# Optimization experiments

Hardware: AMD Instinct MI355X
Metric: run time of the kernel (lower is better)

## Reference

```python
import jax, jax.numpy as jnp
import numpy as np

HEADS = 16
HEAD_DIM = 32
WINDOW = 64  # kernel_size = 2*WINDOW + 1 = 129
NEG = -1e30


def setup_inputs() -> dict:
    key = jax.random.key(0)
    ks = jax.random.split(key, 9)
    B, T, D, G = 4, 8192, HEADS * HEAD_DIM, 64
    x = jax.random.normal(ks[0], (B, T, D), jnp.float32)
    def W(k):
        return jax.random.normal(k, (D, D), jnp.float32) * 0.02
    def b(k):
        return jax.random.normal(k, (D,), jnp.float32) * 0.02
    return {
        "x": x,
        "Wq": W(ks[1]), "bq": b(ks[2]),
        "Wk": W(ks[3]), "bk": b(ks[4]),
        "Wv": W(ks[5]), "bv": b(ks[6]),
        "Wo": W(ks[7]), "bo": b(ks[8]),
        "global_idx": jnp.arange(G, dtype=jnp.int64 if jax.config.jax_enable_x64 else jnp.int32),
    }


def _sparse_global_attn(x, Wq, bq, Wk, bk, Wv, bv, Wo, bo, global_idx):
    B, T, D = x.shape
    H, d, w = HEADS, HEAD_DIM, WINDOW
    scale = 1.0 / (d ** 0.5)

    def proj(W, b):
        # (B,T,D) -> (B,H,T,d)
        return (x @ W + b).reshape(B, T, H, d).transpose(0, 2, 1, 3)

    q, k, v = proj(Wq, bq), proj(Wk, bk), proj(Wv, bv)

    offsets = jnp.arange(-w, w + 1)  # (K,)
    K = offsets.shape[0]

    # Local band scores: score[b,h,t,j] = <q[t], k[t+offset_j]>, computed
    # offset-by-offset via roll to avoid a (B,H,T,K,d) gather.
    def score_step(_, o):
        s = jnp.einsum('bhtd,bhtd->bht', q, jnp.roll(k, -o, axis=2))
        return None, s
    _, loc = jax.lax.scan(score_step, None, offsets)  # (K,B,H,T)
    loc = jnp.moveaxis(loc, 0, -1) * scale            # (B,H,T,K)

    pos = jnp.arange(T)[:, None] + offsets[None, :]   # (T,K)
    valid = (pos >= 0) & (pos < T)
    loc = jnp.where(valid[None, None], loc, NEG)

    # Global-token scores (global tokens shared across the batch)
    k_g = k[:, :, global_idx, :]                      # (B,H,G,d)
    v_g = v[:, :, global_idx, :]
    gsc = jnp.einsum('bhtd,bhgd->bhtg', q, k_g) * scale  # (B,H,T,G)

    # Joint softmax over [local window | global tokens] (duplicates where a
    # global token lies inside the local window, matching the original).
    attn = jax.nn.softmax(jnp.concatenate([loc, gsc], axis=-1), axis=-1)
    a_loc = jnp.moveaxis(attn[..., :K], -1, 0)        # (K,B,H,T)
    a_g = attn[..., K:]                               # (B,H,T,G)

    def ctx_step(acc, oa):
        o, a = oa
        return acc + a[..., None] * jnp.roll(v, -o, axis=2), None
    ctx, _ = jax.lax.scan(ctx_step, jnp.zeros_like(q), (offsets, a_loc))
    ctx = ctx + jnp.einsum('bhtg,bhgd->bhtd', a_g, v_g)  # (B,H,T,d)

    out = ctx.transpose(0, 2, 1, 3).reshape(B, T, D)
    return out @ Wo + bo


def reference(x, Wq, bq, Wk, bk, Wv, bv, Wo, bo, global_idx):
    return _sparse_global_attn(x, Wq, bq, Wk, bk, Wv, bv, Wo, bo, global_idx)
```

## Files before the change

### kernel.cpp

```cpp
#include <hip/hip_runtime.h>
#include <hip/hip_bf16.h>
#include <cstdint>
#include <cstddef>

using bf16 = __hip_bfloat16;
typedef __bf16 bf16x8 __attribute__((ext_vector_type(8)));
typedef __bf16 bf16x4 __attribute__((ext_vector_type(4)));
typedef float f32x4 __attribute__((ext_vector_type(4)));

constexpr int BB = 4;
constexpr int TS = 8192;
constexpr int NH = 16;
constexpr int HD = 32;
constexpr int DM = 512;
constexpr int NQKV = 1536;
constexpr int NG = 64;

#define MFMA16(a, b, c) __builtin_amdgcn_mfma_f32_16x16x32_bf16((a), (b), (c), 0, 0, 0)

__device__ __forceinline__ bf16x8 ld8(const bf16* p) { return *(const bf16x8*)p; }
__device__ __forceinline__ bf16x4 ld4(const bf16* p) { return *(const bf16x4*)p; }
__device__ __forceinline__ unsigned short b16bits(bf16 v) { return __builtin_bit_cast(unsigned short, v); }

__device__ __forceinline__ void gl_lds16(const bf16* g, void* l) {
  __builtin_amdgcn_global_load_lds((const __attribute__((address_space(1))) void*)g,
                                   (__attribute__((address_space(3))) void*)l, 16, 0, 0);
}

__global__ void prep_kernel(const float* __restrict__ x,
                            const float* __restrict__ Wq, const float* __restrict__ bq,
                            const float* __restrict__ Wk, const float* __restrict__ bk,
                            const float* __restrict__ Wv, const float* __restrict__ bv,
                            const float* __restrict__ Wo,
                            bf16* __restrict__ xb, bf16* __restrict__ Wp,
                            bf16* __restrict__ Wp2, float* __restrict__ bqkv) {
  const int64_t stride = (int64_t)gridDim.x * blockDim.x;
  const int64_t i0 = (int64_t)blockIdx.x * blockDim.x + threadIdx.x;
  const float4* x4 = (const float4*)x;
  ushort4* xb4 = (ushort4*)xb;
  for (int64_t i = i0; i < (int64_t)BB * TS * DM / 4; i += stride) {
    float4 v = x4[i];
    ushort4 o;
    o.x = b16bits(__float2bfloat16(v.x));
    o.y = b16bits(__float2bfloat16(v.y));
    o.z = b16bits(__float2bfloat16(v.z));
    o.w = b16bits(__float2bfloat16(v.w));
    xb4[i] = o;
  }
  for (int64_t c = i0; c < (int64_t)NQKV * DM / 8; c += stride) {
    const int lane = (int)(c & 63), f = (int)((c >> 6) & 3), ks = (int)((c >> 8) & 1);
    const int kt = (int)((c >> 9) & 7), wn = (int)((c >> 12) & 1), nt = (int)(c >> 13);
    const int n = nt * 128 + wn * 64 + f * 16 + (lane & 15);
    const int k = kt * 64 + ks * 32 + (lane >> 4) * 8;
    const float* W = (n < 512) ? Wq : ((n < 1024) ? Wk : Wv);
    const int nn = n & 511;
    #pragma unroll
    for (int j = 0; j < 8; ++j)
      Wp[c * 8 + j] = __float2bfloat16(W[(size_t)(k + j) * DM + nn]);
  }
  for (int64_t c = i0; c < (int64_t)DM * DM / 8; c += stride) {
    const int lane = (int)(c & 63), f = (int)((c >> 6) & 3), ks = (int)((c >> 8) & 1);
    const int kt = (int)((c >> 9) & 7), wn = (int)((c >> 12) & 1), nt = (int)(c >> 13);
    const int n = nt * 128 + wn * 64 + f * 16 + (lane & 15);
    const int k = kt * 64 + ks * 32 + (lane >> 4) * 8;
    #pragma unroll
    for (int j = 0; j < 8; ++j)
      Wp2[c * 8 + j] = __float2bfloat16(Wo[(size_t)(k + j) * DM + n]);
  }
  for (int64_t i = i0; i < NQKV; i += stride)
    bqkv[i] = (i < 512) ? bq[i] : ((i < 1024) ? bk[i - 512] : bv[i - 1024]);
}

template <bool F32OUT, bool WVT>
__global__ __launch_bounds__(256, 3) void gemm_bias(const bf16* __restrict__ A,
                                                    const bf16* __restrict__ Bp,
                                                    const float* __restrict__ bias,
                                                    void* __restrict__ Cv,
                                                    bf16* __restrict__ vt,
                                                    int M, int N, int K, int cpx) {
  __shared__ __attribute__((aligned(16))) char smem[35072];
  const int tid = threadIdx.x;
  const int lane = tid & 63, wid = tid >> 6;
  const int grp = lane >> 4, col = lane & 15;
  const int bid = (blockIdx.x & 7) * cpx + (blockIdx.x >> 3);
  const int NT = N >> 7;
  const int mt = bid / NT, nt = bid % NT;
  const int m0 = mt << 7, n0 = nt << 7;
  const int wm = wid >> 1, wn = wid & 1;
  const int KT = K >> 6;
  f32x4 acc[4][4] = {};

  const bf16* bp = Bp + (size_t)(nt * 2 + wn) * KT * 4096 + lane * 8;
  bf16x8 breg[2][4];
  auto loadB = [&](int kt) {
    #pragma unroll
    for (int ks = 0; ks < 2; ++ks)
      #pragma unroll
      for (int f = 0; f < 4; ++f)
        breg[ks][f] = ld8(bp + (size_t)(kt * 8 + ks * 4 + f) * 512);
  };
  auto stageA = [&](int kt) {
    char* buf = smem + (kt & 1) * 16384;
    #pragma unroll
    for (int c = 0; c < 4; ++c) {
      const int chunk = wid * 4 + c;
      const int row = chunk * 8 + (lane >> 3);
      const int sl = lane & 7;
      const int koff = ((sl ^ (row & 7)) << 3) + (kt << 6);
      gl_lds16(A + (size_t)(m0 + row) * K + koff, buf + chunk * 1024);
    }
  };

  stageA(0);
  loadB(0);
  for (int kt = 0; kt < KT; ++kt) {
    if (kt + 1 < KT) {
      stageA(kt + 1);
      __builtin_amdgcn_sched_barrier(0);
      asm volatile("s_waitcnt vmcnt(4)" ::: "memory");
    } else {
      __builtin_amdgcn_sched_barrier(0);
      asm volatile("s_waitcnt vmcnt(0)" ::: "memory");
    }
    __builtin_amdgcn_sched_barrier(0);
    __builtin_amdgcn_s_barrier();
    __builtin_amdgcn_sched_barrier(0);
    const char* sA = smem + (kt & 1) * 16384;
    #pragma unroll
    for (int ks = 0; ks < 2; ++ks) {
      bf16x8 af[4];
      #pragma unroll
      for (int f = 0; f < 4; ++f) {
        const int ra = wm * 64 + f * 16 + col;
        af[f] = *(const bf16x8*)(sA + ra * 128 + (((ks * 4 + grp) ^ (ra & 7)) << 4));
      }
      #pragma unroll
      for (int i = 0; i < 4; ++i)
        #pragma unroll
        for (int j = 0; j < 4; ++j)
          acc[i][j] = MFMA16(af[i], breg[ks][j], acc[i][j]);
    }
    if (kt + 1 < KT) loadB(kt + 1);
    __builtin_amdgcn_sched_barrier(0);
    __builtin_amdgcn_s_barrier();
    __builtin_amdgcn_sched_barrier(0);
  }

  const bool wv = WVT && (n0 >= 1024);
  if (!wv) {
    #pragma unroll
    for (int i = 0; i < 4; ++i)
      #pragma unroll
      for (int j = 0; j < 4; ++j) {
        const int n = n0 + wn * 64 + j * 16 + col;
        const float bz = bias[n];
        #pragma unroll
        for (int r = 0; r < 4; ++r) {
          const int m = m0 + wm * 64 + i * 16 + grp * 4 + r;
          const float v = acc[i][j][r] + bz;
          if (F32OUT)
            ((float*)Cv)[(size_t)m * N + n] = v;
          else
            ((bf16*)Cv)[(size_t)m * N + n] = __float2bfloat16(v);
        }
      }
  } else {
    __syncthreads();
    bf16* lt = (bf16*)smem;
    #pragma unroll
    for (int i = 0; i < 4; ++i)
      #pragma unroll
      for (int j = 0; j < 4; ++j) {
        const int nl = wn * 64 + j * 16 + col;
        const float bz = bias[n0 + nl];
        #pragma unroll
        for (int r = 0; r < 4; ++r) {
          const int ml = wm * 64 + i * 16 + grp * 4 + r;
          lt[nl * 136 + (ml ^ ((nl & 7) << 4))] = __float2bfloat16(acc[i][j][r] + bz);
        }
      }
    __syncthreads();
    const int row = tid >> 1, half = tid & 1;
    const int b = m0 >> 13, t0 = m0 & 8191;
    bf16* dst = vt + (size_t)(b * DM + (n0 & 511) + row) * TS + t0 + half * 64;
    const bf16* srcl = lt + row * 136;
    #pragma unroll
    for (int c = 0; c < 8; ++c)
      *(bf16x8*)(dst + c * 8) =
          *(const bf16x8*)(srcl + ((half * 64 + c * 8) ^ ((row & 7) << 4)));
  }
}

__global__ void vgt_kernel(const bf16* __restrict__ vt, const int* __restrict__ gidx,
                           bf16* __restrict__ vtp, bf16* __restrict__ vgt) {
  const int64_t stride = (int64_t)gridDim.x * blockDim.x;
  const int64_t i0 = (int64_t)blockIdx.x * blockDim.x + threadIdx.x;
  for (int64_t i = i0; i < 512; i += stride) {
    if (i < 64) vtp[i - 64] = __float2bfloat16(0.f);
    else vtp[(size_t)2048 * TS + (i - 64)] = __float2bfloat16(0.f);
  }
  for (int64_t i = i0; i < (int64_t)2048 * NG; i += stride) {
    const int row = (int)(i >> 6), g = (int)(i & 63);
    const int gi = gidx[g];
    vgt[i] = vt[(size_t)row * TS + gi];
  }
}

__global__ __launch_bounds__(256) void attn_kernel(const bf16* __restrict__ qkv,
                                                   const bf16* __restrict__ vt,
                                                   const bf16* __restrict__ vgt,
                                                   const int* __restrict__ gidx,
                                                   bf16* __restrict__ ctx) {
  constexpr int VST = 216;
  constexpr int VGST = 88;
  __shared__ __attribute__((aligned(16))) char smem[35840];
  bf16* sV = (bf16*)smem;
  bf16* sVg = (bf16*)(smem + 13824);
  bf16* sK = (bf16*)(smem + 19456);
  bf16* sKg = (bf16*)(smem + 31744);

  const int tid = threadIdx.x, wid = tid >> 6, lane = tid & 63;
  const int grp = lane >> 4, col = lane & 15;
  const int bid = (blockIdx.x & 7) * 1024 + (blockIdx.x >> 3);
  const int tile = bid & 127, h = (bid >> 7) & 15, b = bid >> 11;
  const int t0b = tile * 64;
  const int kbb = t0b - 64;
  const int bh = b * NH + h;
  const bf16* base = qkv + (size_t)b * TS * NQKV;
  const bf16* kpl = base + 512 + h * 32;

  #pragma unroll
  for (int it = 0; it < 3; ++it) {
    const int idx = it * 256 + tid;
    const int row = idx >> 2, part = idx & 3;
    const int tok = min(max(kbb + row, 0), TS - 1);
    gl_lds16(kpl + (size_t)tok * NQKV + ((part ^ (row & 3)) << 3), sK + idx * 8);
  }
  {
    const int row = tid >> 2, part = tid & 3;
    const int gi = gidx[row];
    gl_lds16(kpl + (size_t)gi * NQKV + ((part ^ (row & 3)) << 3), sKg + tid * 8);
  }
  {
    const bf16* vr = vt + (size_t)(bh * HD + (tid >> 3)) * TS + kbb;
    #pragma unroll
    for (int i = 0; i < 4; ++i) {
      const int c = i * 8 + (tid & 7);
      if (c < 27) *(bf16x8*)(sV + (tid >> 3) * VST + c * 8) = ld8(vr + c * 8);
    }
  }
  {
    const int row = tid >> 3, c = tid & 7;
    *(bf16x8*)(sVg + row * VGST + c * 8) = ld8(vgt + (size_t)(bh * HD + row) * NG + c * 8);
  }
  __syncthreads();

  const int qt = t0b + wid * 16;
  const int offw = wid * 16;

  const bf16x8 qf = ld8(base + (size_t)(qt + col) * NQKV + h * 32 + grp * 8);
  const f32x4 z = {0.f, 0.f, 0.f, 0.f};
  f32x4 s[13];
  #pragma unroll
  for (int f = 0; f < 9; ++f) {
    const int row = offw + f * 16 + col;
    bf16x8 kf = ld8(sK + row * 32 + ((grp ^ (row & 3)) << 3));
    s[f] = MFMA16(kf, qf, z);
  }
  #pragma unroll
  for (int f = 0; f < 4; ++f) {
    const int row = f * 16 + col;
    bf16x8 kf = ld8(sKg + row * 32 + ((grp ^ (row & 3)) << 3));
    s[9 + f] = MFMA16(kf, qf, z);
  }
  const float scale = 0.17677669529663688f;
  float mx = -3e38f;
  const bool interior = (tile >= 1) & (tile <= 126);
  if (interior) {
    #pragma unroll
    for (int f = 0; f < 13; ++f) {
      #pragma unroll
      for (int r = 0; r < 4; ++r) {
        float v = s[f][r] * scale;
        if (f == 0) v = (grp * 4 + r >= col) ? v : -1e30f;
        if (f == 8) v = (grp * 4 + r <= col) ? v : -1e30f;
        s[f][r] = v;
        mx = fmaxf(mx, v);
      }
    }
  } else {
    #pragma unroll
    for (int f = 0; f < 13; ++f) {
      #pragma unroll
      for (int r = 0; r < 4; ++r) {
        float v = s[f][r] * scale;
        if (f < 9) {
          const int j = f * 16 + grp * 4 + r;
          const int pos = qt - 64 + j;
          const bool valid = (j >= col) & (j <= col + 128) & (pos >= 0) & (pos < TS);
          v = valid ? v : -1e30f;
        }
        s[f][r] = v;
        mx = fmaxf(mx, v);
      }
    }
  }
  mx = fmaxf(mx, __shfl_xor(mx, 16));
  mx = fmaxf(mx, __shfl_xor(mx, 32));
  float sum = 0.f;
  bf16x8 pb[7];
  #pragma unroll
  for (int f = 0; f < 13; ++f) {
    const int pr = (f < 9) ? (f >> 1) : (5 + ((f - 9) >> 1));
    const int hf = (f < 9) ? (f & 1) : ((f - 9) & 1);
    #pragma unroll
    for (int r = 0; r < 4; ++r) {
      float p = __expf(s[f][r] - mx);
      sum += p;
      pb[pr][hf * 4 + r] = (__bf16)__float2bfloat16(p);
    }
  }
  #pragma unroll
  for (int r = 0; r < 4; ++r) pb[4][4 + r] = (__bf16)__float2bfloat16(0.f);
  sum += __shfl_xor(sum, 16);
  sum += __shfl_xor(sum, 32);
  const float sm = 1.0f / sum;

  f32x4 c0 = z, c1 = z;
  const bf16* sVr0 = sV + col * VST;
  const bf16* sVr1 = sV + (col + 16) * VST;
  #pragma unroll
  for (int i = 0; i < 5; ++i) {
    const int kk = offw + i * 32 + grp * 4;
    bf16x8 a0 = __builtin_shufflevector(ld4(sVr0 + kk), ld4(sVr0 + kk + 16),
                                        0, 1, 2, 3, 4, 5, 6, 7);
    bf16x8 a1 = __builtin_shufflevector(ld4(sVr1 + kk), ld4(sVr1 + kk + 16),
                                        0, 1, 2, 3, 4, 5, 6, 7);
    c0 = MFMA16(a0, pb[i], c0);
    c1 = MFMA16(a1, pb[i], c1);
  }
  const bf16* sVg0 = sVg + col * VGST;
  const bf16* sVg1 = sVg + (col + 16) * VGST;
  #pragma unroll
  for (int i = 0; i < 2; ++i) {
    const int kk = i * 32 + grp * 4;
    bf16x8 a0 = __builtin_shufflevector(ld4(sVg0 + kk), ld4(sVg0 + kk + 16),
                                        0, 1, 2, 3, 4, 5, 6, 7);
    bf16x8 a1 = __builtin_shufflevector(ld4(sVg1 + kk), ld4(sVg1 + kk + 16),
                                        0, 1, 2, 3, 4, 5, 6, 7);
    c0 = MFMA16(a0, pb[5 + i], c0);
    c1 = MFMA16(a1, pb[5 + i], c1);
  }
  const int t = qt + col;
  bf16* op = ctx + ((size_t)(b * TS + t)) * DM + h * 32 + grp * 4;
  ushort4 o0, o1;
  o0.x = b16bits(__float2bfloat16(c0[0] * sm));
  o0.y = b16bits(__float2bfloat16(c0[1] * sm));
  o0.z = b16bits(__float2bfloat16(c0[2] * sm));
  o0.w = b16bits(__float2bfloat16(c0[3] * sm));
  o1.x = b16bits(__float2bfloat16(c1[0] * sm));
  o1.y = b16bits(__float2bfloat16(c1[1] * sm));
  o1.z = b16bits(__float2bfloat16(c1[2] * sm));
  o1.w = b16bits(__float2bfloat16(c1[3] * sm));
  *(ushort4*)op = o0;
  *(ushort4*)(op + 16) = o1;
}

extern "C" void kernel_launch(void* const* d_in, const int* in_sizes, int n_in,
                              void* d_out, int out_size, void* d_ws, size_t ws_size,
                              hipStream_t stream) {
  (void)in_sizes; (void)n_in; (void)out_size; (void)ws_size;
  const float* x = (const float*)d_in[0];
  const float* Wq = (const float*)d_in[1];
  const float* bq = (const float*)d_in[2];
  const float* Wk = (const float*)d_in[3];
  const float* bk = (const float*)d_in[4];
  const float* Wv = (const float*)d_in[5];
  const float* bv = (const float*)d_in[6];
  const float* Wo = (const float*)d_in[7];
  const float* bo = (const float*)d_in[8];
  const int* gidx = (const int*)d_in[9];
  float* out = (float*)d_out;

  char* ws = (char*)d_ws;
  size_t off = 0;
  auto alloc = [&](size_t bytes) -> void* {
    void* p = ws + off;
    off += (bytes + 255) & ~(size_t)255;
    return p;
  };
  bf16* xb = (bf16*)alloc((size_t)BB * TS * DM * 2);
  bf16* Wp = (bf16*)alloc((size_t)NQKV * DM * 2);
  bf16* Wp2 = (bf16*)alloc((size_t)DM * DM * 2);
  float* bqkv = (float*)alloc((size_t)NQKV * 4);
  bf16* qkv = (bf16*)alloc((size_t)BB * TS * NQKV * 2);
  bf16* vta = (bf16*)alloc(((size_t)2048 * TS + 512) * 2);
  bf16* vgt = (bf16*)alloc((size_t)2048 * NG * 2);
  bf16* ctx = xb;
  bf16* vt = vta + 64;

  prep_kernel<<<dim3(2048), dim3(256), 0, stream>>>(x, Wq, bq, Wk, bk, Wv, bv, Wo,
                                                    xb, Wp, Wp2, bqkv);
  gemm_bias<false, true><<<dim3(3072), dim3(256), 0, stream>>>(xb, Wp, bqkv, qkv, vt,
                                                               BB * TS, NQKV, DM, 384);
  vgt_kernel<<<dim3(512), dim3(256), 0, stream>>>(vt, gidx, vt, vgt);
  attn_kernel<<<dim3(8192), dim3(256), 0, stream>>>(qkv, vt, vgt, gidx, ctx);
  gemm_bias<true, false><<<dim3(1024), dim3(256), 0, stream>>>(ctx, Wp2, bo, out, nullptr,
                                                               BB * TS, DM, DM, 128);
}
```

Baseline: 168.0 us.

## Restructure projection GEMMs to 64x512 tiles with full-K A staged in LDS

The projection GEMMs change from 128x128 tiles with double-buffered K-chunks to 64-row by 512-column tiles. Each 512-thread block stages the entire 64x512 A panel into LDS once, then each of eight waves streams its own B columns from global memory, with register double-buffering over 16 k-steps. The weight prepacking layout is changed to match the new per-wave column groups, and the V-transpose epilogue is split into two passes. This cuts A re-reads and per-k barriers, at the cost of 64KB LDS per block, which may limit occupancy, and more B traffic per output.

Result: slower. 194.0 us (+15.5%).

```diff
diff --git a/kernel.cpp b/kernel.cpp
--- a/kernel.cpp
+++ b/kernel.cpp
@@ -49,8 +49,8 @@
   }
   for (int64_t c = i0; c < (int64_t)NQKV * DM / 8; c += stride) {
     const int lane = (int)(c & 63), f = (int)((c >> 6) & 3), ks = (int)((c >> 8) & 1);
-    const int kt = (int)((c >> 9) & 7), wn = (int)((c >> 12) & 1), nt = (int)(c >> 13);
-    const int n = nt * 128 + wn * 64 + f * 16 + (lane & 15);
+    const int kt = (int)((c >> 9) & 7), g = (int)(c >> 12);
+    const int n = g * 64 + f * 16 + (lane & 15);
     const int k = kt * 64 + ks * 32 + (lane >> 4) * 8;
     const float* W = (n < 512) ? Wq : ((n < 1024) ? Wk : Wv);
     const int nn = n & 511;
@@ -60,8 +60,8 @@
   }
   for (int64_t c = i0; c < (int64_t)DM * DM / 8; c += stride) {
     const int lane = (int)(c & 63), f = (int)((c >> 6) & 3), ks = (int)((c >> 8) & 1);
-    const int kt = (int)((c >> 9) & 7), wn = (int)((c >> 12) & 1), nt = (int)(c >> 13);
-    const int n = nt * 128 + wn * 64 + f * 16 + (lane & 15);
+    const int kt = (int)((c >> 9) & 7), g = (int)(c >> 12);
+    const int n = g * 64 + f * 16 + (lane & 15);
     const int k = kt * 64 + ks * 32 + (lane >> 4) * 8;
     #pragma unroll
     for (int j = 0; j < 8; ++j)
@@ -71,123 +71,124 @@
     bqkv[i] = (i < 512) ? bq[i] : ((i < 1024) ? bk[i - 512] : bv[i - 1024]);
 }
 
-template <bool F32OUT, bool WVT>
-__global__ __launch_bounds__(256, 3) void gemm_bias(const bf16* __restrict__ A,
+template <bool F32OUT, bool WVT, int NTB>
+__global__ __launch_bounds__(512, 4) void gemm_bias(const bf16* __restrict__ A,
                                                     const bf16* __restrict__ Bp,
                                                     const float* __restrict__ bias,
                                                     void* __restrict__ Cv,
                                                     bf16* __restrict__ vt,
-                                                    int M, int N, int K, int cpx) {
-  __shared__ __attribute__((aligned(16))) char smem[35072];
+                                                    int M, int N, int cpx) {
+  __shared__ __attribute__((aligned(16))) char smem[65536];
   const int tid = threadIdx.x;
   const int lane = tid & 63, wid = tid >> 6;
   const int grp = lane >> 4, col = lane & 15;
   const int bid = (blockIdx.x & 7) * cpx + (blockIdx.x >> 3);
-  const int NT = N >> 7;
-  const int mt = bid / NT, nt = bid % NT;
-  const int m0 = mt << 7, n0 = nt << 7;
-  const int wm = wid >> 1, wn = wid & 1;
-  const int KT = K >> 6;
+  const int mt = bid / NTB, nt = bid % NTB;
+  const int m0 = mt << 6, n0 = nt << 9;
   f32x4 acc[4][4] = {};
 
-  const bf16* bp = Bp + (size_t)(nt * 2 + wn) * KT * 4096 + lane * 8;
-  bf16x8 breg[2][4];
-  auto loadB = [&](int kt) {
-    #pragma unroll
-    for (int ks = 0; ks < 2; ++ks)
-      #pragma unroll
-      for (int f = 0; f < 4; ++f)
-        breg[ks][f] = ld8(bp + (size_t)(kt * 8 + ks * 4 + f) * 512);
-  };
-  auto stageA = [&](int kt) {
-    char* buf = smem + (kt & 1) * 16384;
-    #pragma unroll
-    for (int c = 0; c < 4; ++c) {
-      const int chunk = wid * 4 + c;
-      const int row = chunk * 8 + (lane >> 3);
-      const int sl = lane & 7;
-      const int koff = ((sl ^ (row & 7)) << 3) + (kt << 6);
-      gl_lds16(A + (size_t)(m0 + row) * K + koff, buf + chunk * 1024);
-    }
-  };
-
-  stageA(0);
-  loadB(0);
-  for (int kt = 0; kt < KT; ++kt) {
-    if (kt + 1 < KT) {
-      stageA(kt + 1);
-      __builtin_amdgcn_sched_barrier(0);
-      asm volatile("s_waitcnt vmcnt(4)" ::: "memory");
-    } else {
-      __builtin_amdgcn_sched_barrier(0);
-      asm volatile("s_waitcnt vmcnt(0)" ::: "memory");
-    }
-    __builtin_amdgcn_sched_barrier(0);
-    __builtin_amdgcn_s_barrier();
-    __builtin_amdgcn_sched_barrier(0);
-    const char* sA = smem + (kt & 1) * 16384;
-    #pragma unroll
-    for (int ks = 0; ks < 2; ++ks) {
+  #pragma unroll
+  for (int it = 0; it < 8; ++it) {
+    const int idx = it * 512 + tid;
+    const int row = idx >> 6, c = idx & 63;
+    const int kt = c >> 3, sl = c & 7;
+    const int koff = kt * 64 + ((sl ^ (row & 7)) << 3);
+    gl_lds16(A + (size_t)(m0 + row) * 512 + koff, smem + idx * 16);
+  }
+  __syncthreads();
+
+  const bf16* bp = Bp + (size_t)(nt * 8 + wid) * 32768 + lane * 8;
+  bf16x8 bA[4], bB[4];
+  #pragma unroll
+  for (int f = 0; f < 4; ++f) bA[f] = ld8(bp + (size_t)f * 512);
+
+  #pragma unroll
+  for (int s = 0; s < 16; s += 2) {
+    if (s + 1 < 16)
+      #pragma unroll
+      for (int f = 0; f < 4; ++f) bB[f] = ld8(bp + (size_t)((s + 1) * 4 + f) * 512);
+    {
+      const int kt = s >> 1, ks = s & 1;
       bf16x8 af[4];
       #pragma unroll
       for (int f = 0; f < 4; ++f) {
-        const int ra = wm * 64 + f * 16 + col;
-        af[f] = *(const bf16x8*)(sA + ra * 128 + (((ks * 4 + grp) ^ (ra & 7)) << 4));
+        const int ra = f * 16 + col;
+        af[f] = *(const bf16x8*)(smem + ra * 1024 + kt * 128 +
+                                 (((ks * 4 + grp) ^ (ra & 7)) << 4));
       }
       #pragma unroll
       for (int i = 0; i < 4; ++i)
         #pragma unroll
         for (int j = 0; j < 4; ++j)
-          acc[i][j] = MFMA16(af[i], breg[ks][j], acc[i][j]);
-    }
-    if (kt + 1 < KT) loadB(kt + 1);
-    __builtin_amdgcn_sched_barrier(0);
-    __builtin_amdgcn_s_barrier();
-    __builtin_amdgcn_sched_barrier(0);
-  }
-
-  const bool wv = WVT && (n0 >= 1024);
+          acc[i][j] = MFMA16(af[i], bA[j], acc[i][j]);
+    }
+    if (s + 2 < 16)
+      #pragma unroll
+      for (int f = 0; f < 4; ++f) bA[f] = ld8(bp + (size_t)((s + 2) * 4 + f) * 512);
+    if (s + 1 < 16) {
+      const int kt = (s + 1) >> 1, ks = (s + 1) & 1;
+      bf16x8 af[4];
+      #pragma unroll
+      for (int f = 0; f < 4; ++f) {
+        const int ra = f * 16 + col;
+        af[f] = *(const bf16x8*)(smem + ra * 1024 + kt * 128 +
+                                 (((ks * 4 + grp) ^ (ra & 7)) << 4));
+      }
+      #pragma unroll
+      for (int i = 0; i < 4; ++i)
+        #pragma unroll
+        for (int j = 0; j < 4; ++j)
+          acc[i][j] = MFMA16(af[i], bB[j], acc[i][j]);
+    }
+  }
+
+  const bool wv = WVT && (nt == 2);
   if (!wv) {
     #pragma unroll
-    for (int i = 0; i < 4; ++i)
-      #pragma unroll
-      for (int j = 0; j < 4; ++j) {
-        const int n = n0 + wn * 64 + j * 16 + col;
-        const float bz = bias[n];
+    for (int j = 0; j < 4; ++j) {
+      const int n = n0 + wid * 64 + j * 16 + col;
+      const float bz = bias[n];
+      #pragma unroll
+      for (int i = 0; i < 4; ++i)
         #pragma unroll
         for (int r = 0; r < 4; ++r) {
-          const int m = m0 + wm * 64 + i * 16 + grp * 4 + r;
+          const int m = m0 + i * 16 + grp * 4 + r;
           const float v = acc[i][j][r] + bz;
           if (F32OUT)
             ((float*)Cv)[(size_t)m * N + n] = v;
           else
             ((bf16*)Cv)[(size_t)m * N + n] = __float2bfloat16(v);
         }
-      }
+    }
   } else {
-    __syncthreads();
     bf16* lt = (bf16*)smem;
-    #pragma unroll
-    for (int i = 0; i < 4; ++i)
-      #pragma unroll
-      for (int j = 0; j < 4; ++j) {
-        const int nl = wn * 64 + j * 16 + col;
-        const float bz = bias[n0 + nl];
+    const int b = m0 >> 13, t0 = m0 & 8191;
+    #pragma unroll
+    for (int p = 0; p < 2; ++p) {
+      __syncthreads();
+      if ((wid >> 2) == p) {
         #pragma unroll
-        for (int r = 0; r < 4; ++r) {
-          const int ml = wm * 64 + i * 16 + grp * 4 + r;
-          lt[nl * 136 + (ml ^ ((nl & 7) << 4))] = __float2bfloat16(acc[i][j][r] + bz);
+        for (int j = 0; j < 4; ++j) {
+          const int nl = (wid & 3) * 64 + j * 16 + col;
+          const float bz = bias[n0 + p * 256 + nl];
+          #pragma unroll
+          for (int i = 0; i < 4; ++i)
+            #pragma unroll
+            for (int r = 0; r < 4; ++r) {
+              const int ml = i * 16 + grp * 4 + r;
+              lt[nl * 72 + (ml ^ ((nl & 7) << 3))] = __float2bfloat16(acc[i][j][r] + bz);
+            }
         }
       }
-    __syncthreads();
-    const int row = tid >> 1, half = tid & 1;
-    const int b = m0 >> 13, t0 = m0 & 8191;
-    bf16* dst = vt + (size_t)(b * DM + (n0 & 511) + row) * TS + t0 + half * 64;
-    const bf16* srcl = lt + row * 136;
-    #pragma unroll
-    for (int c = 0; c < 8; ++c)
-      *(bf16x8*)(dst + c * 8) =
-          *(const bf16x8*)(srcl + ((half * 64 + c * 8) ^ ((row & 7) << 4)));
+      __syncthreads();
+      const int row = tid >> 1, half = tid & 1;
+      bf16* dst = vt + (size_t)(b * DM + p * 256 + row) * TS + t0 + half * 32;
+      const bf16* srcl = lt + row * 72;
+      #pragma unroll
+      for (int c = 0; c < 4; ++c)
+        *(bf16x8*)(dst + c * 8) =
+            *(const bf16x8*)(srcl + ((half * 32 + c * 8) ^ ((row & 7) << 3)));
+    }
   }
 }
 
@@ -401,10 +402,10 @@
 
   prep_kernel<<<dim3(2048), dim3(256), 0, stream>>>(x, Wq, bq, Wk, bk, Wv, bv, Wo,
                                                     xb, Wp, Wp2, bqkv);
-  gemm_bias<false, true><<<dim3(3072), dim3(256), 0, stream>>>(xb, Wp, bqkv, qkv, vt,
-                                                               BB * TS, NQKV, DM, 384);
+  gemm_bias<false, true, 3><<<dim3(1536), dim3(512), 0, stream>>>(
+      xb, Wp, bqkv, qkv, vt, BB * TS, NQKV, 192);
   vgt_kernel<<<dim3(512), dim3(256), 0, stream>>>(vt, gidx, vt, vgt);
   attn_kernel<<<dim3(8192), dim3(256), 0, stream>>>(qkv, vt, vgt, gidx, ctx);
-  gemm_bias<true, false><<<dim3(1024), dim3(256), 0, stream>>>(ctx, Wp2, bo, out, nullptr,
-                                                               BB * TS, DM, DM, 128);
-}
+  gemm_bias<true, false, 1><<<dim3(512), dim3(512), 0, stream>>>(
+      ctx, Wp2, bo, out, nullptr, BB * TS, DM, 64);
+}
```

## Triple-buffer A tiles and double-buffer B registers in GEMM pipeline

Applied to the files above, without the earlier changes.

The GEMM mainloop moves from a double-buffered A tile in LDS to a three-stage ring. A is prefetched two iterations ahead, and B fragments are double-buffered in registers so the next B load is issued before the MFMAs. K is fixed at compile time so the loop fully unrolls, and s_setprio is raised around the MFMA block. The prep-kernel weight packing index math is simplified (g = c>>12), which gives the same layout. LDS grows to 48KB and register use rises, which could lower occupancy under launch_bounds(256,3).

Result: slower. 212.6 us (+26.5%).

```diff
diff --git a/kernel.cpp b/kernel.cpp
--- a/kernel.cpp
+++ b/kernel.cpp
@@ -49,8 +49,8 @@
   }
   for (int64_t c = i0; c < (int64_t)NQKV * DM / 8; c += stride) {
     const int lane = (int)(c & 63), f = (int)((c >> 6) & 3), ks = (int)((c >> 8) & 1);
-    const int kt = (int)((c >> 9) & 7), wn = (int)((c >> 12) & 1), nt = (int)(c >> 13);
-    const int n = nt * 128 + wn * 64 + f * 16 + (lane & 15);
+    const int kt = (int)((c >> 9) & 7), g = (int)(c >> 12);
+    const int n = g * 64 + f * 16 + (lane & 15);
     const int k = kt * 64 + ks * 32 + (lane >> 4) * 8;
     const float* W = (n < 512) ? Wq : ((n < 1024) ? Wk : Wv);
     const int nn = n & 511;
@@ -60,8 +60,8 @@
   }
   for (int64_t c = i0; c < (int64_t)DM * DM / 8; c += stride) {
     const int lane = (int)(c & 63), f = (int)((c >> 6) & 3), ks = (int)((c >> 8) & 1);
-    const int kt = (int)((c >> 9) & 7), wn = (int)((c >> 12) & 1), nt = (int)(c >> 13);
-    const int n = nt * 128 + wn * 64 + f * 16 + (lane & 15);
+    const int kt = (int)((c >> 9) & 7), g = (int)(c >> 12);
+    const int n = g * 64 + f * 16 + (lane & 15);
     const int k = kt * 64 + ks * 32 + (lane >> 4) * 8;
     #pragma unroll
     for (int j = 0; j < 8; ++j)
@@ -77,8 +77,8 @@
                                                     const float* __restrict__ bias,
                                                     void* __restrict__ Cv,
                                                     bf16* __restrict__ vt,
-                                                    int M, int N, int K, int cpx) {
-  __shared__ __attribute__((aligned(16))) char smem[35072];
+                                                    int M, int N, int cpx) {
+  __shared__ __attribute__((aligned(16))) char smem[49152];
   const int tid = threadIdx.x;
   const int lane = tid & 63, wid = tid >> 6;
   const int grp = lane >> 4, col = lane & 15;
@@ -87,60 +87,66 @@
   const int mt = bid / NT, nt = bid % NT;
   const int m0 = mt << 7, n0 = nt << 7;
   const int wm = wid >> 1, wn = wid & 1;
-  const int KT = K >> 6;
+  constexpr int KT = 8;
   f32x4 acc[4][4] = {};
 
-  const bf16* bp = Bp + (size_t)(nt * 2 + wn) * KT * 4096 + lane * 8;
-  bf16x8 breg[2][4];
-  auto loadB = [&](int kt) {
-    #pragma unroll
-    for (int ks = 0; ks < 2; ++ks)
-      #pragma unroll
-      for (int f = 0; f < 4; ++f)
-        breg[ks][f] = ld8(bp + (size_t)(kt * 8 + ks * 4 + f) * 512);
-  };
-  auto stageA = [&](int kt) {
-    char* buf = smem + (kt & 1) * 16384;
+  const bf16* bp = Bp + (size_t)(nt * 2 + wn) * (KT * 4096) + lane * 8;
+  bf16x8 brg[2][2][4];
+
+  auto stageA = [&](int kt, int buf3) {
+    char* buf = smem + buf3 * 16384;
     #pragma unroll
     for (int c = 0; c < 4; ++c) {
       const int chunk = wid * 4 + c;
       const int row = chunk * 8 + (lane >> 3);
       const int sl = lane & 7;
       const int koff = ((sl ^ (row & 7)) << 3) + (kt << 6);
-      gl_lds16(A + (size_t)(m0 + row) * K + koff, buf + chunk * 1024);
+      gl_lds16(A + (size_t)(m0 + row) * 512 + koff, buf + chunk * 1024);
     }
   };
 
-  stageA(0);
-  loadB(0);
+  stageA(0, 0);
+  #pragma unroll
+  for (int ks = 0; ks < 2; ++ks)
+    #pragma unroll
+    for (int f = 0; f < 4; ++f)
+      brg[0][ks][f] = ld8(bp + (size_t)(ks * 4 + f) * 512);
+  stageA(1, 1);
+
+  #pragma unroll
   for (int kt = 0; kt < KT; ++kt) {
-    if (kt + 1 < KT) {
-      stageA(kt + 1);
-      __builtin_amdgcn_sched_barrier(0);
-      asm volatile("s_waitcnt vmcnt(4)" ::: "memory");
-    } else {
-      __builtin_amdgcn_sched_barrier(0);
-      asm volatile("s_waitcnt vmcnt(0)" ::: "memory");
-    }
+    __builtin_amdgcn_sched_barrier(0);
+    if (kt + 1 < KT) asm volatile("s_waitcnt vmcnt(4)" ::: "memory");
+    else             asm volatile("s_waitcnt vmcnt(0)" ::: "memory");
     __builtin_amdgcn_sched_barrier(0);
     __builtin_amdgcn_s_barrier();
     __builtin_amdgcn_sched_barrier(0);
-    const char* sA = smem + (kt & 1) * 16384;
-    #pragma unroll
-    for (int ks = 0; ks < 2; ++ks) {
-      bf16x8 af[4];
+    const char* sA = smem + (kt % 3) * 16384;
+    bf16x8 af[2][4];
+    #pragma unroll
+    for (int ks = 0; ks < 2; ++ks)
       #pragma unroll
       for (int f = 0; f < 4; ++f) {
         const int ra = wm * 64 + f * 16 + col;
-        af[f] = *(const bf16x8*)(sA + ra * 128 + (((ks * 4 + grp) ^ (ra & 7)) << 4));
+        af[ks][f] = *(const bf16x8*)(sA + ra * 128 + (((ks * 4 + grp) ^ (ra & 7)) << 4));
       }
+    if (kt + 1 < KT) {
+      #pragma unroll
+      for (int ks = 0; ks < 2; ++ks)
+        #pragma unroll
+        for (int f = 0; f < 4; ++f)
+          brg[(kt + 1) & 1][ks][f] = ld8(bp + (size_t)((kt + 1) * 8 + ks * 4 + f) * 512);
+    }
+    __builtin_amdgcn_s_setprio(1);
+    #pragma unroll
+    for (int ks = 0; ks < 2; ++ks)
       #pragma unroll
       for (int i = 0; i < 4; ++i)
         #pragma unroll
         for (int j = 0; j < 4; ++j)
-          acc[i][j] = MFMA16(af[i], breg[ks][j], acc[i][j]);
-    }
-    if (kt + 1 < KT) loadB(kt + 1);
+          acc[i][j] = MFMA16(af[ks][i], brg[kt & 1][ks][j], acc[i][j]);
+    __builtin_amdgcn_s_setprio(0);
+    if (kt + 2 < KT) stageA(kt + 2, (kt + 2) % 3);
     __builtin_amdgcn_sched_barrier(0);
     __builtin_amdgcn_s_barrier();
     __builtin_amdgcn_sched_barrier(0);
@@ -402,9 +408,9 @@
   prep_kernel<<<dim3(2048), dim3(256), 0, stream>>>(x, Wq, bq, Wk, bk, Wv, bv, Wo,
                                                     xb, Wp, Wp2, bqkv);
   gemm_bias<false, true><<<dim3(3072), dim3(256), 0, stream>>>(xb, Wp, bqkv, qkv, vt,
-                                                               BB * TS, NQKV, DM, 384);
+                                                               BB * TS, NQKV, 384);
   vgt_kernel<<<dim3(512), dim3(256), 0, stream>>>(vt, gidx, vt, vgt);
   attn_kernel<<<dim3(8192), dim3(256), 0, stream>>>(qkv, vt, vgt, gidx, ctx);
   gemm_bias<true, false><<<dim3(1024), dim3(256), 0, stream>>>(ctx, Wp2, bo, out, nullptr,
-                                                               BB * TS, DM, DM, 128);
-}
+                                                               BB * TS, DM, 128);
+}
```

## Fuse fp32-to-bf16 conversion of x into QKV GEMM A-tile loading

Applied to the files above, without the earlier changes.

Removes the separate pass that converts x to bf16 in the prep kernel. The QKV GEMM now reads fp32 x straight into registers, converts it, and writes swizzled bf16 tiles to LDS with a register-prefetch pipeline. The K dimension is fixed at compile time so the loops fully unroll, and setprio is raised around the MFMA block. This saves a full read and write of x, but the GEMM now reads each fp32 A tile once per N tile (12 times), which costs more global bandwidth and register pressure.

Result: slower. 468.2 us (+178.6%).

```diff
diff --git a/kernel.cpp b/kernel.cpp
--- a/kernel.cpp
+++ b/kernel.cpp
@@ -27,30 +27,18 @@
                                    (__attribute__((address_space(3))) void*)l, 16, 0, 0);
 }
 
-__global__ void prep_kernel(const float* __restrict__ x,
-                            const float* __restrict__ Wq, const float* __restrict__ bq,
+__global__ void prep_kernel(const float* __restrict__ Wq, const float* __restrict__ bq,
                             const float* __restrict__ Wk, const float* __restrict__ bk,
                             const float* __restrict__ Wv, const float* __restrict__ bv,
                             const float* __restrict__ Wo,
-                            bf16* __restrict__ xb, bf16* __restrict__ Wp,
-                            bf16* __restrict__ Wp2, float* __restrict__ bqkv) {
+                            bf16* __restrict__ Wp, bf16* __restrict__ Wp2,
+                            float* __restrict__ bqkv) {
   const int64_t stride = (int64_t)gridDim.x * blockDim.x;
   const int64_t i0 = (int64_t)blockIdx.x * blockDim.x + threadIdx.x;
-  const float4* x4 = (const float4*)x;
-  ushort4* xb4 = (ushort4*)xb;
-  for (int64_t i = i0; i < (int64_t)BB * TS * DM / 4; i += stride) {
-    float4 v = x4[i];
-    ushort4 o;
-    o.x = b16bits(__float2bfloat16(v.x));
-    o.y = b16bits(__float2bfloat16(v.y));
-    o.z = b16bits(__float2bfloat16(v.z));
-    o.w = b16bits(__float2bfloat16(v.w));
-    xb4[i] = o;
-  }
   for (int64_t c = i0; c < (int64_t)NQKV * DM / 8; c += stride) {
     const int lane = (int)(c & 63), f = (int)((c >> 6) & 3), ks = (int)((c >> 8) & 1);
-    const int kt = (int)((c >> 9) & 7), wn = (int)((c >> 12) & 1), nt = (int)(c >> 13);
-    const int n = nt * 128 + wn * 64 + f * 16 + (lane & 15);
+    const int kt = (int)((c >> 9) & 7), g = (int)(c >> 12);
+    const int n = g * 64 + f * 16 + (lane & 15);
     const int k = kt * 64 + ks * 32 + (lane >> 4) * 8;
     const float* W = (n < 512) ? Wq : ((n < 1024) ? Wk : Wv);
     const int nn = n & 511;
@@ -60,8 +48,8 @@
   }
   for (int64_t c = i0; c < (int64_t)DM * DM / 8; c += stride) {
     const int lane = (int)(c & 63), f = (int)((c >> 6) & 3), ks = (int)((c >> 8) & 1);
-    const int kt = (int)((c >> 9) & 7), wn = (int)((c >> 12) & 1), nt = (int)(c >> 13);
-    const int n = nt * 128 + wn * 64 + f * 16 + (lane & 15);
+    const int kt = (int)((c >> 9) & 7), g = (int)(c >> 12);
+    const int n = g * 64 + f * 16 + (lane & 15);
     const int k = kt * 64 + ks * 32 + (lane >> 4) * 8;
     #pragma unroll
     for (int j = 0; j < 8; ++j)
@@ -71,13 +59,13 @@
     bqkv[i] = (i < 512) ? bq[i] : ((i < 1024) ? bk[i - 512] : bv[i - 1024]);
 }
 
-template <bool F32OUT, bool WVT>
-__global__ __launch_bounds__(256, 3) void gemm_bias(const bf16* __restrict__ A,
+template <bool F32A, bool F32OUT, bool WVT>
+__global__ __launch_bounds__(256, 3) void gemm_bias(const void* __restrict__ Av,
                                                     const bf16* __restrict__ Bp,
                                                     const float* __restrict__ bias,
                                                     void* __restrict__ Cv,
                                                     bf16* __restrict__ vt,
-                                                    int M, int N, int K, int cpx) {
+                                                    int M, int N, int cpx) {
   __shared__ __attribute__((aligned(16))) char smem[35072];
   const int tid = threadIdx.x;
   const int lane = tid & 63, wid = tid >> 6;
@@ -87,10 +75,10 @@
   const int mt = bid / NT, nt = bid % NT;
   const int m0 = mt << 7, n0 = nt << 7;
   const int wm = wid >> 1, wn = wid & 1;
-  const int KT = K >> 6;
+  constexpr int KT = 8;
   f32x4 acc[4][4] = {};
 
-  const bf16* bp = Bp + (size_t)(nt * 2 + wn) * KT * 4096 + lane * 8;
+  const bf16* bp = Bp + (size_t)(nt * 2 + wn) * (KT * 4096) + lane * 8;
   bf16x8 breg[2][4];
   auto loadB = [&](int kt) {
     #pragma unroll
@@ -99,51 +87,126 @@
       for (int f = 0; f < 4; ++f)
         breg[ks][f] = ld8(bp + (size_t)(kt * 8 + ks * 4 + f) * 512);
   };
-  auto stageA = [&](int kt) {
-    char* buf = smem + (kt & 1) * 16384;
-    #pragma unroll
-    for (int c = 0; c < 4; ++c) {
-      const int chunk = wid * 4 + c;
-      const int row = chunk * 8 + (lane >> 3);
-      const int sl = lane & 7;
-      const int koff = ((sl ^ (row & 7)) << 3) + (kt << 6);
-      gl_lds16(A + (size_t)(m0 + row) * K + koff, buf + chunk * 1024);
-    }
-  };
-
-  stageA(0);
-  loadB(0);
-  for (int kt = 0; kt < KT; ++kt) {
-    if (kt + 1 < KT) {
-      stageA(kt + 1);
-      __builtin_amdgcn_sched_barrier(0);
-      asm volatile("s_waitcnt vmcnt(4)" ::: "memory");
-    } else {
-      __builtin_amdgcn_sched_barrier(0);
-      asm volatile("s_waitcnt vmcnt(0)" ::: "memory");
-    }
+
+  if constexpr (!F32A) {
+    const bf16* A = (const bf16*)Av;
+    auto stageA = [&](int kt) {
+      char* buf = smem + (kt & 1) * 16384;
+      #pragma unroll
+      for (int c = 0; c < 4; ++c) {
+        const int chunk = wid * 4 + c;
+        const int row = chunk * 8 + (lane >> 3);
+        const int sl = lane & 7;
+        const int koff = ((sl ^ (row & 7)) << 3) + (kt << 6);
+        gl_lds16(A + (size_t)(m0 + row) * 512 + koff, buf + chunk * 1024);
+      }
+    };
+    stageA(0);
+    loadB(0);
+    #pragma unroll
+    for (int kt = 0; kt < KT; ++kt) {
+      if (kt + 1 < KT) {
+        stageA(kt + 1);
+        __builtin_amdgcn_sched_barrier(0);
+        asm volatile("s_waitcnt vmcnt(4)" ::: "memory");
+      } else {
+        __builtin_amdgcn_sched_barrier(0);
+        asm volatile("s_waitcnt vmcnt(0)" ::: "memory");
+      }
+      __builtin_amdgcn_sched_barrier(0);
+      __builtin_amdgcn_s_barrier();
+      __builtin_amdgcn_sched_barrier(0);
+      const char* sA = smem + (kt & 1) * 16384;
+      #pragma unroll
+      for (int ks = 0; ks < 2; ++ks) {
+        bf16x8 af[4];
+        #pragma unroll
+        for (int f = 0; f < 4; ++f) {
+          const int ra = wm * 64 + f * 16 + col;
+          af[f] = *(const bf16x8*)(sA + ra * 128 + (((ks * 4 + grp) ^ (ra & 7)) << 4));
+        }
+        #pragma unroll
+        for (int i = 0; i < 4; ++i)
+          #pragma unroll
+          for (int j = 0; j < 4; ++j)
+            acc[i][j] = MFMA16(af[i], breg[ks][j], acc[i][j]);
+      }
+      if (kt + 1 < KT) loadB(kt + 1);
+      __builtin_amdgcn_sched_barrier(0);
+      __builtin_amdgcn_s_barrier();
+      __builtin_amdgcn_sched_barrier(0);
+    }
+  } else {
+    const float* Af = (const float*)Av;
+    f32x4 rA[8];
+    auto loadA = [&](int kt) {
+      #pragma unroll
+      for (int i = 0; i < 8; ++i) {
+        const int idx = i * 256 + tid;
+        const int row = idx >> 4, c16 = idx & 15;
+        rA[i] = *(const f32x4*)(Af + (size_t)(m0 + row) * 512 + (kt << 6) + (c16 << 2));
+      }
+    };
+    auto writeA = [&](int d) {
+      char* buf = smem + d * 16384;
+      #pragma unroll
+      for (int i = 0; i < 8; ++i) {
+        const int idx = i * 256 + tid;
+        const int row = idx >> 4, c16 = idx & 15;
+        bf16x4 w;
+        w[0] = (__bf16)__float2bfloat16(rA[i][0]);
+        w[1] = (__bf16)__float2bfloat16(rA[i][1]);
+        w[2] = (__bf16)__float2bfloat16(rA[i][2]);
+        w[3] = (__bf16)__float2bfloat16(rA[i][3]);
+        *(bf16x4*)(buf + row * 128 + (((c16 >> 1) ^ (row & 7)) << 4) +
+                   ((c16 & 1) << 3)) = w;
+      }
+    };
+    loadA(0);
+    loadB(0);
+    asm volatile("s_waitcnt vmcnt(8)" ::: "memory");
+    writeA(0);
+    loadA(1);
+    asm volatile("s_waitcnt lgkmcnt(0)" ::: "memory");
     __builtin_amdgcn_sched_barrier(0);
     __builtin_amdgcn_s_barrier();
     __builtin_amdgcn_sched_barrier(0);
-    const char* sA = smem + (kt & 1) * 16384;
-    #pragma unroll
-    for (int ks = 0; ks < 2; ++ks) {
-      bf16x8 af[4];
-      #pragma unroll
-      for (int f = 0; f < 4; ++f) {
-        const int ra = wm * 64 + f * 16 + col;
-        af[f] = *(const bf16x8*)(sA + ra * 128 + (((ks * 4 + grp) ^ (ra & 7)) << 4));
-      }
-      #pragma unroll
-      for (int i = 0; i < 4; ++i)
-        #pragma unroll
-        for (int j = 0; j < 4; ++j)
-          acc[i][j] = MFMA16(af[i], breg[ks][j], acc[i][j]);
-    }
-    if (kt + 1 < KT) loadB(kt + 1);
-    __builtin_amdgcn_sched_barrier(0);
-    __builtin_amdgcn_s_barrier();
-    __builtin_amdgcn_sched_barrier(0);
+    #pragma unroll
+    for (int kt = 0; kt < KT; ++kt) {
+      const char* sA = smem + (kt & 1) * 16384;
+      bf16x8 af[2][4];
+      #pragma unroll
+      for (int ks = 0; ks < 2; ++ks)
+        #pragma unroll
+        for (int f = 0; f < 4; ++f) {
+          const int ra = wm * 64 + f * 16 + col;
+          af[ks][f] = *(const bf16x8*)(sA + ra * 128 + (((ks * 4 + grp) ^ (ra & 7)) << 4));
+        }
+      __builtin_amdgcn_sched_barrier(0);
+      if (kt + 1 < KT) asm volatile("s_waitcnt vmcnt(8)" ::: "memory");
+      else             asm volatile("s_waitcnt vmcnt(0)" ::: "memory");
+      __builtin_amdgcn_sched_barrier(0);
+      __builtin_amdgcn_s_setprio(1);
+      #pragma unroll
+      for (int ks = 0; ks < 2; ++ks)
+        #pragma unroll
+        for (int i = 0; i < 4; ++i)
+          #pragma unroll
+          for (int j = 0; j < 4; ++j)
+            acc[i][j] = MFMA16(af[ks][i], breg[ks][j], acc[i][j]);
+      __builtin_amdgcn_s_setprio(0);
+      if (kt + 1 < KT) {
+        loadB(kt + 1);
+        __builtin_amdgcn_sched_barrier(0);
+        asm volatile("s_waitcnt vmcnt(8)" ::: "memory");
+        writeA((kt + 1) & 1);
+        if (kt + 2 < KT) loadA(kt + 2);
+      }
+      asm volatile("s_waitcnt lgkmcnt(0)" ::: "memory");
+      __builtin_amdgcn_sched_barrier(0);
+      __builtin_amdgcn_s_barrier();
+      __builtin_amdgcn_sched_barrier(0);
+    }
   }
 
   const bool wv = WVT && (n0 >= 1024);
@@ -389,22 +452,21 @@
     off += (bytes + 255) & ~(size_t)255;
     return p;
   };
-  bf16* xb = (bf16*)alloc((size_t)BB * TS * DM * 2);
+  bf16* ctx = (bf16*)alloc((size_t)BB * TS * DM * 2);
   bf16* Wp = (bf16*)alloc((size_t)NQKV * DM * 2);
   bf16* Wp2 = (bf16*)alloc((size_t)DM * DM * 2);
   float* bqkv = (float*)alloc((size_t)NQKV * 4);
   bf16* qkv = (bf16*)alloc((size_t)BB * TS * NQKV * 2);
   bf16* vta = (bf16*)alloc(((size_t)2048 * TS + 512) * 2);
   bf16* vgt = (bf16*)alloc((size_t)2048 * NG * 2);
-  bf16* ctx = xb;
   bf16* vt = vta + 64;
 
-  prep_kernel<<<dim3(2048), dim3(256), 0, stream>>>(x, Wq, bq, Wk, bk, Wv, bv, Wo,
-                                                    xb, Wp, Wp2, bqkv);
-  gemm_bias<false, true><<<dim3(3072), dim3(256), 0, stream>>>(xb, Wp, bqkv, qkv, vt,
-                                                               BB * TS, NQKV, DM, 384);
+  prep_kernel<<<dim3(512), dim3(256), 0, stream>>>(Wq, bq, Wk, bk, Wv, bv, Wo,
+                                                   Wp, Wp2, bqkv);
+  gemm_bias<true, false, true><<<dim3(3072), dim3(256), 0, stream>>>(
+      x, Wp, bqkv, qkv, vt, BB * TS, NQKV, 384);
   vgt_kernel<<<dim3(512), dim3(256), 0, stream>>>(vt, gidx, vt, vgt);
   attn_kernel<<<dim3(8192), dim3(256), 0, stream>>>(qkv, vt, vgt, gidx, ctx);
-  gemm_bias<true, false><<<dim3(1024), dim3(256), 0, stream>>>(ctx, Wp2, bo, out, nullptr,
-                                                               BB * TS, DM, DM, 128);
-}
+  gemm_bias<false, true, false><<<dim3(1024), dim3(256), 0, stream>>>(
+      ctx, Wp2, bo, out, nullptr, BB * TS, DM, 128);
+}
```
